# Kernel tuning notes

Measured on AMD Instinct MI355X. Metric: run time of the kernel, lower is better.

Reference implementation:

```python
import jax, jax.numpy as jnp
import numpy as np

BS, NQ, D = 4, 12500, 256
HEADS, LEVELS, POINTS = 8, 2, 4
HD = D // HEADS
D_FF = 2048
SHAPES = ((100, 100), (50, 50))   # (H, W) per level; sum(H*W) == NQ
STARTS = (0, 10000)


def layer_norm(x, g, b, eps=1e-5):
    m = x.mean(-1, keepdims=True)
    v = ((x - m) ** 2).mean(-1, keepdims=True)
    return (x - m) * jax.lax.rsqrt(v + eps) * g + b


def bilinear_sample(value_l, loc, H, W):
    # value_l: (bs, heads, H*W, hd); loc: (bs, heads, nq, P, 2) normalized [0,1]
    # matches F.grid_sample(align_corners=False, padding_mode='zeros')
    x = loc[..., 0] * W - 0.5
    y = loc[..., 1] * H - 0.5
    x0 = jnp.floor(x)
    y0 = jnp.floor(y)
    wx1 = x - x0
    wy1 = y - y0
    wx0 = 1.0 - wx1
    wy0 = 1.0 - wy1
    x0i = x0.astype(jnp.int32)
    y0i = y0.astype(jnp.int32)

    def gather(xi, yi):
        valid = (xi >= 0) & (xi < W) & (yi >= 0) & (yi < H)
        idx = jnp.clip(yi, 0, H - 1) * W + jnp.clip(xi, 0, W - 1)  # (bs,heads,nq,P)
        b, h, nq, P = idx.shape
        g = jnp.take_along_axis(value_l, idx.reshape(b, h, nq * P, 1), axis=2)
        g = g.reshape(b, h, nq, P, -1)
        return g * valid[..., None].astype(g.dtype)

    g00 = gather(x0i, y0i)
    g10 = gather(x0i + 1, y0i)
    g01 = gather(x0i, y0i + 1)
    g11 = gather(x0i + 1, y0i + 1)
    return (g00 * (wx0 * wy0)[..., None] + g10 * (wx1 * wy0)[..., None]
            + g01 * (wx0 * wy1)[..., None] + g11 * (wx1 * wy1)[..., None])


def setup_inputs() -> dict:
    key = jax.random.key(0)
    ks = jax.random.split(key, 20)
    s = 0.02
    inp = {
        'query': jax.random.normal(ks[0], (BS, NQ, D), jnp.float32),
        'reference_points': jax.random.uniform(ks[1], (BS, NQ, LEVELS, 2), jnp.float32),
        'w_off': s * jax.random.normal(ks[2], (D, HEADS * LEVELS * POINTS * 2), jnp.float32),
        'b_off': s * jax.random.normal(ks[3], (HEADS * LEVELS * POINTS * 2,), jnp.float32),
        'w_attn': s * jax.random.normal(ks[4], (D, HEADS * LEVELS * POINTS), jnp.float32),
        'b_attn': s * jax.random.normal(ks[5], (HEADS * LEVELS * POINTS,), jnp.float32),
        'w_val': s * jax.random.normal(ks[6], (D, D), jnp.float32),
        'b_val': jnp.zeros((D,), jnp.float32),
        'w_out': s * jax.random.normal(ks[7], (D, D), jnp.float32),
        'b_out': jnp.zeros((D,), jnp.float32),
        'w1': s * jax.random.normal(ks[8], (D, D_FF), jnp.float32),
        'b1': jnp.zeros((D_FF,), jnp.float32),
        'w2': s * jax.random.normal(ks[9], (D_FF, D), jnp.float32),
        'b2': jnp.zeros((D,), jnp.float32),
        'ln0_g': jnp.ones((D,), jnp.float32),
        'ln0_b': jnp.zeros((D,), jnp.float32),
        'ln1_g': jnp.ones((D,), jnp.float32),
        'ln1_b': jnp.zeros((D,), jnp.float32),
    }
    return inp


def reference(query, reference_points, w_off, b_off, w_attn, b_attn, w_val, b_val,
              w_out, b_out, w1, b1, w2, b2, ln0_g, ln0_b, ln1_g, ln1_b):
    bs, nq, _ = query.shape
    # value projection; encoder self-attention: value == query tokens
    value = (query @ w_val + b_val).reshape(bs, nq, HEADS, HD).transpose(0, 2, 1, 3)  # (bs,heads,nv,hd)
    off = (query @ w_off + b_off).reshape(bs, nq, HEADS, LEVELS, POINTS, 2)
    aw = (query @ w_attn + b_attn).reshape(bs, nq, HEADS, LEVELS * POINTS)
    aw = jax.nn.softmax(aw, axis=-1).reshape(bs, nq, HEADS, LEVELS, POINTS)

    out = jnp.zeros((bs, HEADS, nq, HD), query.dtype)
    for l, (H, W) in enumerate(SHAPES):
        normalizer = jnp.array([W, H], query.dtype)
        # (bs,nq,heads,P,2)
        loc = reference_points[:, :, None, l, None, :] + off[:, :, :, l] / normalizer
        loc = loc.transpose(0, 2, 1, 3, 4)  # (bs,heads,nq,P,2)
        v_l = value[:, :, STARTS[l]:STARTS[l] + H * W]  # (bs,heads,H*W,hd)
        sampled = bilinear_sample(v_l, loc, H, W)       # (bs,heads,nq,P,hd)
        w_l = aw[:, :, :, l].transpose(0, 2, 1, 3)      # (bs,heads,nq,P)
        out = out + (sampled * w_l[..., None]).sum(axis=3)

    attn_out = out.transpose(0, 2, 1, 3).reshape(bs, nq, D) @ w_out + b_out
    x = layer_norm(query + attn_out, ln0_g, ln0_b)
    h = jax.nn.relu(x @ w1 + b1)
    x = layer_norm(x + (h @ w2 + b2), ln1_g, ln1_b)
    return x
```

## Files before the change

### kernel.cpp

```cpp
#include <hip/hip_runtime.h>


#define NQv 12500
#define BSv 4
#define Dv  256
#define DFF 2048

typedef __attribute__((ext_vector_type(8))) __bf16 bf16x8;
typedef __attribute__((ext_vector_type(4))) float f32x4;

__device__ __forceinline__ ushort f32_to_bf16(float f) {
  unsigned u = __float_as_uint(f);
  u += 0x7FFFu + ((u >> 16) & 1u);
  return (ushort)(u >> 16);
}
__device__ __forceinline__ float bf16_to_f32(ushort u) {
  return __uint_as_float(((unsigned)u) << 16);
}

__global__ __launch_bounds__(256) void conv_bf16_kernel(
    const float* __restrict__ in, ushort* __restrict__ out, int n4) {
  int i = blockIdx.x * 256 + threadIdx.x;
  if (i >= n4) return;
  float4 v = reinterpret_cast<const float4*>(in)[i];
  uint2 st;
  st.x = (unsigned)f32_to_bf16(v.x) | ((unsigned)f32_to_bf16(v.y) << 16);
  st.y = (unsigned)f32_to_bf16(v.z) | ((unsigned)f32_to_bf16(v.w) << 16);
  reinterpret_cast<uint2*>(out)[i] = st;
}

__global__ __launch_bounds__(256) void ttrans_kernel(
    const float* __restrict__ in, ushort* __restrict__ out, int K, int N) {
  __shared__ ushort tl[64][65];
  const int n0 = blockIdx.x * 64, k0 = blockIdx.y * 64;
  const int t = threadIdx.x;
#pragma unroll
  for (int i = 0; i < 16; ++i) {
    int idx = t + 256 * i;
    int r = idx >> 6, c = idx & 63;
    tl[r][c] = f32_to_bf16(in[(size_t)(k0 + r) * N + n0 + c]);
  }
  __syncthreads();
#pragma unroll
  for (int i = 0; i < 16; ++i) {
    int idx = t + 256 * i;
    int r = idx >> 6, c = idx & 63;
    out[(size_t)(n0 + r) * K + k0 + c] = tl[c][r];
  }
}

__global__ __launch_bounds__(256) void build_wcat_kernel(
    const float* __restrict__ w_val, const float* __restrict__ w_off,
    const float* __restrict__ w_attn, const float* __restrict__ b_val,
    const float* __restrict__ b_off, const float* __restrict__ b_attn,
    ushort* __restrict__ wcat, float* __restrict__ bcat) {
  int i = blockIdx.x * 256 + threadIdx.x;
  if (i < 448 * 256) {
    int n = i >> 8, k = i & 255;
    float v = (n < 256) ? w_val[(size_t)k * 256 + n]
              : (n < 384) ? w_off[(size_t)k * 128 + (n - 256)]
                          : w_attn[(size_t)k * 64 + (n - 384)];
    wcat[i] = f32_to_bf16(v);
  }
  if (i < 512)
    bcat[i] = (i < 256) ? b_val[i] : (i < 384) ? b_off[i - 256]
              : (i < 448) ? b_attn[i - 384] : 0.f;
}

#define TBM 128
#define TBN 128
#define TBK 32

template <int RELU, int NMASK>
__global__ __launch_bounds__(256) void gemm128_kernel(
    const ushort* __restrict__ A, const ushort* __restrict__ Bt,
    const float* __restrict__ bias, ushort* __restrict__ C,
    int M, int K, int ldc, int Nreal) {
  __shared__ ushort lds[4][TBM * TBK];

  const int t = threadIdx.x;
  const int wid = t >> 6, lane = t & 63;
  const int wr = wid >> 1, wc = wid & 1;
  const int m0 = blockIdx.y * TBM;
  const int n0 = blockIdx.x * TBN;

  int srowA[2], srowB[2], gsl[2];
#pragma unroll
  for (int i = 0; i < 2; i++) {
    int row = i * 64 + (t >> 2);
    int ar = m0 + row;
    srowA[i] = (ar < M) ? ar : (M - 1);
    srowB[i] = n0 + row;
    gsl[i] = ((t & 3) ^ ((row >> 1) & 3)) * 8;
  }

  f32x4 acc[4][4] = {};
  const int nt = K / TBK;
  int cur = 0;

#pragma unroll
  for (int i = 0; i < 2; i++) {
    const int ldsoff = (i * 256 + wid * 64) * 8;
    __builtin_amdgcn_global_load_lds(
        (const __attribute__((address_space(1))) void*)(A + (size_t)srowA[i] * K + gsl[i]),
        (__attribute__((address_space(3))) void*)(lds[0] + ldsoff), 16, 0, 0);
    __builtin_amdgcn_global_load_lds(
        (const __attribute__((address_space(1))) void*)(Bt + (size_t)srowB[i] * K + gsl[i]),
        (__attribute__((address_space(3))) void*)(lds[1] + ldsoff), 16, 0, 0);
  }
  __syncthreads();

  const int rl = lane & 15, kh = lane >> 4;
  for (int tk = 0; tk < nt; ++tk) {
    if (tk + 1 < nt) {
      const int k0 = (tk + 1) * TBK;
      const int nb = (cur ^ 1) * 2;
#pragma unroll
      for (int i = 0; i < 2; i++) {
        const int ldsoff = (i * 256 + wid * 64) * 8;
        __builtin_amdgcn_global_load_lds(
            (const __attribute__((address_space(1))) void*)(A + (size_t)srowA[i] * K + k0 + gsl[i]),
            (__attribute__((address_space(3))) void*)(lds[nb] + ldsoff), 16, 0, 0);
        __builtin_amdgcn_global_load_lds(
            (const __attribute__((address_space(1))) void*)(Bt + (size_t)srowB[i] * K + k0 + gsl[i]),
            (__attribute__((address_space(3))) void*)(lds[nb + 1] + ldsoff), 16, 0, 0);
      }
    }
    {
      const ushort* As = lds[cur * 2];
      const ushort* Bs = lds[cur * 2 + 1];
      bf16x8 afr[4], bfr[4];
#pragma unroll
      for (int ni = 0; ni < 4; ni++) {
        int rowb = wc * 64 + ni * 16 + rl;
        int p = kh ^ ((rowb >> 1) & 3);
        bfr[ni] = *reinterpret_cast<const bf16x8*>(Bs + rowb * 32 + p * 8);
      }
#pragma unroll
      for (int mi = 0; mi < 4; mi++) {
        int rowa = wr * 64 + mi * 16 + rl;
        int p = kh ^ ((rowa >> 1) & 3);
        afr[mi] = *reinterpret_cast<const bf16x8*>(As + rowa * 32 + p * 8);
      }
#pragma unroll
      for (int mi = 0; mi < 4; mi++)
#pragma unroll
        for (int ni = 0; ni < 4; ni++)
          acc[mi][ni] = __builtin_amdgcn_mfma_f32_16x16x32_bf16(afr[mi], bfr[ni], acc[mi][ni], 0, 0, 0);
    }
    __syncthreads();
    cur ^= 1;
  }

  ushort* ldsC = lds[0];
  const int rgrp = lane >> 4, cl = lane & 15;
#pragma unroll
  for (int pass = 0; pass < 2; ++pass) {
    if (wr == pass) {
#pragma unroll
      for (int mi = 0; mi < 4; mi++) {
#pragma unroll
        for (int ni = 0; ni < 4; ni++) {
          int col = wc * 64 + ni * 16 + cl;
          float bv = bias[n0 + col];
#pragma unroll
          for (int r = 0; r < 4; r++) {
            int rloc = mi * 16 + rgrp * 4 + r;
            float v = acc[mi][ni][r] + bv;
            if (RELU) v = fmaxf(v, 0.f);
            ldsC[rloc * 132 + col] = f32_to_bf16(v);
          }
        }
      }
    }
    __syncthreads();
    {
      int rloc = t >> 2;
      int row = m0 + pass * 64 + rloc;
      if (row < M) {
#pragma unroll
        for (int j = 0; j < 4; j++) {
          int col = (t & 3) * 32 + j * 8;
          if (!NMASK || n0 + col < Nreal) {
            uint4 v = *reinterpret_cast<const uint4*>(ldsC + rloc * 132 + col);
            *reinterpret_cast<uint4*>(C + (size_t)row * ldc + n0 + col) = v;
          }
        }
      }
    }
    __syncthreads();
  }
}

__global__ __launch_bounds__(256, 2) void ffn_ln_fused_kernel(
    const ushort* __restrict__ xb,
    const ushort* __restrict__ w1t,
    const float* __restrict__ b1,
    const ushort* __restrict__ w2t,
    const float* __restrict__ b2,
    const float* __restrict__ g1, const float* __restrict__ be1,
    float* __restrict__ out,
    int M) {
  __shared__ ushort lds_all[40960];
  ushort* As  = lds_all;
  ushort* Hs  = lds_all + 16384;
  ushort* stg[2] = {lds_all + 24576, lds_all + 32768};
  float* zbuf = (float*)(lds_all + 16384);

  const int t = threadIdx.x;
  const int wv = t >> 6, lane = t & 63;
  const int rl = lane & 15, kq = lane >> 4;
  const int g = lane >> 4, cl = lane & 15;
  const int m0 = blockIdx.x * 64;

  const int r1 = t >> 3;
  const int ls1 = (t & 7) ^ (r1 & 7);
  const int r2 = t >> 2;
  const int ls2 = (t & 3) ^ ((t >> 3) & 3);
  const int rA = t >> 5;
  const int lsA = (t & 31) ^ ((t >> 5) & 7);

#pragma unroll
  for (int ii = 0; ii < 8; ++ii) {
    int row = rA + 8 * ii;
    int ar = m0 + row; ar = (ar < M) ? ar : (M - 1);
    __builtin_amdgcn_global_load_lds(
        (const __attribute__((address_space(1))) void*)(xb + (size_t)ar * 256 + lsA * 8),
        (__attribute__((address_space(3))) void*)(As + (t + 256 * ii) * 8), 16, 0, 0);
  }
#pragma unroll
  for (int ii = 0; ii < 4; ++ii) {
    __builtin_amdgcn_global_load_lds(
        (const __attribute__((address_space(1))) void*)(w1t + (size_t)(r1 + 32 * ii) * 256 + ls1 * 8),
        (__attribute__((address_space(3))) void*)(stg[0] + (t + 256 * ii) * 8), 16, 0, 0);
  }
  __syncthreads();

  auto issue_stage = [&](int i, ushort* dst) {
    int p = i >> 3, j = i & 7;
    if (j < 4) {
      const ushort* gp = w1t + (size_t)(p * 128 + r1) * 256 + j * 64 + ls1 * 8;
#pragma unroll
      for (int ii = 0; ii < 4; ++ii)
        __builtin_amdgcn_global_load_lds(
            (const __attribute__((address_space(1))) void*)(gp + (size_t)ii * 32 * 256),
            (__attribute__((address_space(3))) void*)(dst + (t + 256 * ii) * 8), 16, 0, 0);
    } else {
      const ushort* gp = w2t + (size_t)r2 * 2048 + p * 128 + (j - 4) * 32 + ls2 * 8;
#pragma unroll
      for (int ii = 0; ii < 4; ++ii)
        __builtin_amdgcn_global_load_lds(
            (const __attribute__((address_space(1))) void*)(gp + (size_t)ii * 64 * 2048),
            (__attribute__((address_space(3))) void*)(dst + (t + 256 * ii) * 8), 16, 0, 0);
    }
  };

  f32x4 acc1[4][2] = {};
  f32x4 accF[4][4] = {};
  int cur = 0;

  for (int p = 0; p < 16; ++p) {
#pragma unroll
    for (int j = 0; j < 4; ++j) {
      issue_stage(p * 8 + j + 1, stg[cur ^ 1]);
      const ushort* Bs = stg[cur];
#pragma unroll
      for (int kk = 0; kk < 2; ++kk) {
        bf16x8 afr[4], bfr[2];
        int slotA = j * 8 + kk * 4 + kq;
#pragma unroll
        for (int mi = 0; mi < 4; mi++) {
          int rowa = mi * 16 + rl;
          afr[mi] = *reinterpret_cast<const bf16x8*>(As + rowa * 256 + (slotA ^ (rowa & 7)) * 8);
        }
        int slotB = kk * 4 + kq;
#pragma unroll
        for (int ni = 0; ni < 2; ni++) {
          int rowb = wv * 32 + ni * 16 + rl;
          bfr[ni] = *reinterpret_cast<const bf16x8*>(Bs + rowb * 64 + (slotB ^ (rowb & 7)) * 8);
        }
#pragma unroll
        for (int mi = 0; mi < 4; mi++)
#pragma unroll
          for (int ni = 0; ni < 2; ni++)
            acc1[mi][ni] = __builtin_amdgcn_mfma_f32_16x16x32_bf16(afr[mi], bfr[ni], acc1[mi][ni], 0, 0, 0);
      }
      if (j == 3) {
#pragma unroll
        for (int ni = 0; ni < 2; ni++) {
          int col = wv * 32 + ni * 16 + cl;
          float b1v = b1[p * 128 + col];
#pragma unroll
          for (int mi = 0; mi < 4; mi++) {
#pragma unroll
            for (int r = 0; r < 4; r++) {
              int row = mi * 16 + g * 4 + r;
              float v = fmaxf(acc1[mi][ni][r] + b1v, 0.f);
              int phys = (col >> 3) ^ ((row >> 1) & 7);
              Hs[row * 128 + phys * 8 + (col & 7)] = f32_to_bf16(v);
            }
          }
        }
#pragma unroll
        for (int mi = 0; mi < 4; mi++)
#pragma unroll
          for (int ni = 0; ni < 2; ni++)
            acc1[mi][ni] = (f32x4){0.f, 0.f, 0.f, 0.f};
      }
      __syncthreads();
      cur ^= 1;
    }
#pragma unroll
    for (int tt = 0; tt < 4; ++tt) {
      int i = p * 8 + 4 + tt;
      if (i + 1 < 128) issue_stage(i + 1, stg[cur ^ 1]);
      const ushort* Bs = stg[cur];
      bf16x8 afr[4], bfr[4];
#pragma unroll
      for (int mi = 0; mi < 4; mi++) {
        int rowa = mi * 16 + rl;
        int slot = tt * 4 + kq;
        afr[mi] = *reinterpret_cast<const bf16x8*>(Hs + rowa * 128 + ((slot ^ ((rowa >> 1) & 7))) * 8);
      }
#pragma unroll
      for (int ni = 0; ni < 4; ni++) {
        int rowb = wv * 64 + ni * 16 + rl;
        bfr[ni] = *reinterpret_cast<const bf16x8*>(Bs + rowb * 32 + ((kq ^ ((rowb >> 1) & 3))) * 8);
      }
#pragma unroll
      for (int mi = 0; mi < 4; mi++)
#pragma unroll
        for (int ni = 0; ni < 4; ni++)
          accF[mi][ni] = __builtin_amdgcn_mfma_f32_16x16x32_bf16(afr[mi], bfr[ni], accF[mi][ni], 0, 0, 0);
      __syncthreads();
      cur ^= 1;
    }
  }

#pragma unroll
  for (int half = 0; half < 2; ++half) {
#pragma unroll
    for (int mm = 0; mm < 2; ++mm) {
      int mi = half * 2 + mm;
#pragma unroll
      for (int ni = 0; ni < 4; ni++) {
        int col = wv * 64 + ni * 16 + cl;
        float b2v = b2[col];
#pragma unroll
        for (int r = 0; r < 4; r++) {
          int rloc = mm * 16 + g * 4 + r;
          zbuf[rloc * 260 + col] = accF[mi][ni][r] + b2v;
        }
      }
    }
    __syncthreads();
#pragma unroll
    for (int it = 0; it < 8; ++it) {
      int rloc = wv * 8 + it;
      int rowt = half * 32 + rloc;
      float4 zv = *reinterpret_cast<const float4*>(&zbuf[rloc * 260 + lane * 4]);
      int phys = (lane >> 1) ^ (rowt & 7);
      const ushort* xp = As + rowt * 256 + phys * 8 + (lane & 1) * 4;
      float x0 = zv.x + bf16_to_f32(xp[0]);
      float x1 = zv.y + bf16_to_f32(xp[1]);
      float x2 = zv.z + bf16_to_f32(xp[2]);
      float x3 = zv.w + bf16_to_f32(xp[3]);
      float s = x0 + x1 + x2 + x3;
      float sq = x0 * x0 + x1 * x1 + x2 * x2 + x3 * x3;
#pragma unroll
      for (int o = 1; o < 64; o <<= 1) {
        s += __shfl_xor(s, o, 64);
        sq += __shfl_xor(sq, o, 64);
      }
      float mean = s * (1.f / 256.f);
      float var = sq * (1.f / 256.f) - mean * mean;
      float rs = rsqrtf(var + 1e-5f);
      float4 gv = *reinterpret_cast<const float4*>(g1 + lane * 4);
      float4 bv = *reinterpret_cast<const float4*>(be1 + lane * 4);
      float4 o4;
      o4.x = (x0 - mean) * rs * gv.x + bv.x;
      o4.y = (x1 - mean) * rs * gv.y + bv.y;
      o4.z = (x2 - mean) * rs * gv.z + bv.z;
      o4.w = (x3 - mean) * rs * gv.w + bv.w;
      int grow = m0 + rowt;
      if (grow < M)
        *reinterpret_cast<float4*>(out + (size_t)grow * 256 + lane * 4) = o4;
    }
    __syncthreads();
  }
}

__global__ __launch_bounds__(256) void deform_attn_kernel(
    const ushort* __restrict__ pcat, const float* __restrict__ refp,
    ushort* __restrict__ out, int total) {
  int tid = blockIdx.x * 256 + threadIdx.x;
  if (tid >= total) return;
  int c0 = (tid & 3) * 8;
  int idx = tid >> 2;
  int h = idx & 7;
  int row = idx >> 3;
  int bl = row / NQv;

  const ushort* prow = pcat + (size_t)row * 448;

  ushort awr[8];
  *reinterpret_cast<uint4*>(awr) = *reinterpret_cast<const uint4*>(prow + 384 + h * 8);
  float lg[8], mx = -1e30f;
#pragma unroll
  for (int i = 0; i < 8; i++) { lg[i] = bf16_to_f32(awr[i]); mx = fmaxf(mx, lg[i]); }
  float ssum = 0.f;
#pragma unroll
  for (int i = 0; i < 8; i++) { lg[i] = __expf(lg[i] - mx); ssum += lg[i]; }
  float inv = 1.f / ssum;

  ushort ofr[16];
  *reinterpret_cast<uint4*>(ofr)     = *reinterpret_cast<const uint4*>(prow + 256 + h * 16);
  *reinterpret_cast<uint4*>(ofr + 8) = *reinterpret_cast<const uint4*>(prow + 256 + h * 16 + 8);
  float4 rp = *reinterpret_cast<const float4*>(refp + (size_t)row * 4);

  float acc8[8] = {};
  const int Ws[2] = {100, 50}, Hs2[2] = {100, 50}, Ss[2] = {0, 10000};
#pragma unroll
  for (int l = 0; l < 2; l++) {
    const int W = Ws[l], H = Hs2[l];
    float fx = (l ? rp.z : rp.x) * (float)W - 0.5f;
    float fy = (l ? rp.w : rp.y) * (float)H - 0.5f;
    const ushort* vbase = pcat + ((size_t)bl * NQv + Ss[l]) * 448 + h * 32 + c0;
#pragma unroll
    for (int p = 0; p < 4; p++) {
      float x = fx + bf16_to_f32(ofr[l * 8 + p * 2 + 0]);
      float y = fy + bf16_to_f32(ofr[l * 8 + p * 2 + 1]);
      float x0f = floorf(x), y0f = floorf(y);
      float wx1 = x - x0f, wy1 = y - y0f;
      float wx0 = 1.f - wx1, wy0 = 1.f - wy1;
      int x0 = (int)x0f, y0 = (int)y0f;
      float aw = lg[l * 4 + p] * inv;

      float cw[4] = {aw * wx0 * wy0, aw * wx1 * wy0, aw * wx0 * wy1, aw * wx1 * wy1};
      int cx[4] = {x0, x0 + 1, x0, x0 + 1};
      int cy[4] = {y0, y0, y0 + 1, y0 + 1};
#pragma unroll
      for (int c = 0; c < 4; c++) {
        int xi = cx[c], yi = cy[c];
        if (xi >= 0 && xi < W && yi >= 0 && yi < H) {
          ushort vr[8];
          *reinterpret_cast<uint4*>(vr) =
              *reinterpret_cast<const uint4*>(vbase + (size_t)(yi * W + xi) * 448);
          float w = cw[c];
#pragma unroll
          for (int j = 0; j < 8; j++) acc8[j] += w * bf16_to_f32(vr[j]);
        }
      }
    }
  }

  ushort st[8];
#pragma unroll
  for (int j = 0; j < 8; j++) st[j] = f32_to_bf16(acc8[j]);
  *reinterpret_cast<uint4*>(out + (size_t)row * 256 + h * 32 + c0) =
      *reinterpret_cast<uint4*>(st);
}

__global__ __launch_bounds__(256) void ln0_kernel(
    const float* __restrict__ A, const ushort* __restrict__ B,
    const float* __restrict__ gamma, const float* __restrict__ beta,
    ushort* __restrict__ outb, int M) {
  int row = blockIdx.x * 4 + (threadIdx.x >> 6);
  int lane = threadIdx.x & 63;
  if (row >= M) return;
  size_t base = (size_t)row * 256 + lane * 4;
  float4 a = *reinterpret_cast<const float4*>(A + base);
  uint2 braw = *reinterpret_cast<const uint2*>(B + base);
  float x0 = a.x + bf16_to_f32((ushort)(braw.x & 0xffffu));
  float x1 = a.y + bf16_to_f32((ushort)(braw.x >> 16));
  float x2 = a.z + bf16_to_f32((ushort)(braw.y & 0xffffu));
  float x3 = a.w + bf16_to_f32((ushort)(braw.y >> 16));
  float s = x0 + x1 + x2 + x3;
  float sq = x0 * x0 + x1 * x1 + x2 * x2 + x3 * x3;
#pragma unroll
  for (int o = 1; o < 64; o <<= 1) {
    s += __shfl_xor(s, o, 64);
    sq += __shfl_xor(sq, o, 64);
  }
  float mean = s * (1.f / 256.f);
  float var = sq * (1.f / 256.f) - mean * mean;
  float rs = rsqrtf(var + 1e-5f);
  float4 gv = *reinterpret_cast<const float4*>(gamma + lane * 4);
  float4 bv = *reinterpret_cast<const float4*>(beta + lane * 4);
  float o0 = (x0 - mean) * rs * gv.x + bv.x;
  float o1 = (x1 - mean) * rs * gv.y + bv.y;
  float o2 = (x2 - mean) * rs * gv.z + bv.z;
  float o3 = (x3 - mean) * rs * gv.w + bv.w;
  uint2 st;
  st.x = (unsigned)f32_to_bf16(o0) | ((unsigned)f32_to_bf16(o1) << 16);
  st.y = (unsigned)f32_to_bf16(o2) | ((unsigned)f32_to_bf16(o3) << 16);
  *reinterpret_cast<uint2*>(outb + base) = st;
}

extern "C" void kernel_launch(void* const* d_in, const int* in_sizes, int n_in,
                              void* d_out, int out_size, void* d_ws, size_t ws_size,
                              hipStream_t stream) {
  const float* query  = (const float*)d_in[0];
  const float* refp   = (const float*)d_in[1];
  const float* w_off  = (const float*)d_in[2];
  const float* b_off  = (const float*)d_in[3];
  const float* w_attn = (const float*)d_in[4];
  const float* b_attn = (const float*)d_in[5];
  const float* w_val  = (const float*)d_in[6];
  const float* b_val  = (const float*)d_in[7];
  const float* w_out  = (const float*)d_in[8];
  const float* b_out  = (const float*)d_in[9];
  const float* w1     = (const float*)d_in[10];
  const float* b1     = (const float*)d_in[11];
  const float* w2     = (const float*)d_in[12];
  const float* b2     = (const float*)d_in[13];
  const float* ln0g   = (const float*)d_in[14];
  const float* ln0b   = (const float*)d_in[15];
  const float* ln1g   = (const float*)d_in[16];
  const float* ln1b   = (const float*)d_in[17];
  float* outp = (float*)d_out;

  char* ws = (char*)d_ws;
  size_t woff = 0;
  auto walloc = [&](size_t bytes) { size_t r = woff; woff += (bytes + 255) & ~(size_t)255; return r; };
  ushort* wcat = (ushort*)(ws + walloc((size_t)512 * 256 * 2));
  float*  bcat = (float*)(ws + walloc(512 * 4));
  ushort* wqt  = (ushort*)(ws + walloc((size_t)256 * 256 * 2));
  ushort* w1t  = (ushort*)(ws + walloc((size_t)DFF * 256 * 2));
  ushort* w2t  = (ushort*)(ws + walloc((size_t)256 * DFF * 2));
  char* arena = ws + woff;
  size_t arena_sz = (ws_size > woff) ? (ws_size - woff) : 0;

  int nb = ((size_t)BSv * NQv * 1920 + (1u << 20) <= arena_sz) ? BSv : 1;
  const int R = nb * NQv;
  ushort* qb   = (ushort*)arena;
  ushort* pcat = (ushort*)(arena + (size_t)R * 512);
  ushort* samp = (ushort*)(arena + (size_t)R * 1408);
  ushort* proj = qb;
  ushort* xb   = samp;

  build_wcat_kernel<<<dim3(448), dim3(256), 0, stream>>>(
      w_val, w_off, w_attn, b_val, b_off, b_attn, wcat, bcat);
  ttrans_kernel<<<dim3(4, 4), dim3(256), 0, stream>>>(w_out, wqt, Dv, Dv);
  ttrans_kernel<<<dim3(DFF / 64, 4), dim3(256), 0, stream>>>(w1, w1t, Dv, DFF);
  ttrans_kernel<<<dim3(4, DFF / 64), dim3(256), 0, stream>>>(w2, w2t, DFF, Dv);

  const int MT = (R + TBM - 1) / TBM;

  for (int c = 0; c < BSv / nb; c++) {
    const int row0 = c * R;
    const float* qrow = query + (size_t)row0 * Dv;

    conv_bf16_kernel<<<dim3((R * 64 + 255) / 256), dim3(256), 0, stream>>>(qrow, qb, R * 64);

    gemm128_kernel<0, 1><<<dim3(4, MT), dim3(256), 0, stream>>>(
        qb, wcat, bcat, pcat, R, Dv, 448, 448);

    deform_attn_kernel<<<dim3((R * 32 + 255) / 256), dim3(256), 0, stream>>>(
        pcat, refp + (size_t)row0 * 4, samp, R * 32);

    gemm128_kernel<0, 0><<<dim3(2, MT), dim3(256), 0, stream>>>(
        samp, wqt, b_out, proj, R, Dv, 256, 256);

    ln0_kernel<<<dim3((R + 3) / 4), dim3(256), 0, stream>>>(qrow, proj, ln0g, ln0b, xb, R);

    ffn_ln_fused_kernel<<<dim3((R + 63) / 64), dim3(256), 0, stream>>>(
        xb, w1t, b1, w2t, b2, ln1g, ln1b, outp + (size_t)row0 * 256, R);
  }
}
```

Measured before the change: 339.7 us.

## Restructure fused FFN kernel to 128-row tiles with triple-buffered weight staging

```diff
diff --git a/kernel.cpp b/kernel.cpp
--- a/kernel.cpp
+++ b/kernel.cpp
@@ -192,7 +192,7 @@
   }
 }
 
-__global__ __launch_bounds__(256, 2) void ffn_ln_fused_kernel(
+__global__ __launch_bounds__(512, 1) void ffn_ln_fused_kernel(
     const ushort* __restrict__ xb,
     const ushort* __restrict__ w1t,
     const float* __restrict__ b1,
@@ -201,59 +201,59 @@
     const float* __restrict__ g1, const float* __restrict__ be1,
     float* __restrict__ out,
     int M) {
-  __shared__ ushort lds_all[40960];
-  ushort* As  = lds_all;
-  ushort* Hs  = lds_all + 16384;
-  ushort* stg[2] = {lds_all + 24576, lds_all + 32768};
-  float* zbuf = (float*)(lds_all + 16384);
+  __shared__ ushort lds_all[74752];
+  ushort* As = lds_all;
+  ushort* Hs = lds_all + 32768;
+  ushort* stg0 = lds_all + 50176;
 
   const int t = threadIdx.x;
-  const int wv = t >> 6, lane = t & 63;
+  const int wv = t >> 6;
+  const int wm = wv >> 2;
+  const int wn = wv & 3;
+  const int lane = t & 63;
   const int rl = lane & 15, kq = lane >> 4;
-  const int g = lane >> 4, cl = lane & 15;
-  const int m0 = blockIdx.x * 64;
-
-  const int r1 = t >> 3;
-  const int ls1 = (t & 7) ^ (r1 & 7);
-  const int r2 = t >> 2;
-  const int ls2 = (t & 3) ^ ((t >> 3) & 3);
-  const int rA = t >> 5;
-  const int lsA = (t & 31) ^ ((t >> 5) & 7);
+  const int cl = lane & 15, g4 = lane >> 4;
+  const int m0 = blockIdx.x * 128;
+
+  const int b1row = t >> 3, b1slot = t & 7;
+  const int b2row = t >> 2, b2slot = t & 3;
+
+  auto stg = [&](int i) { return stg0 + i * 8192; };
+
+  auto issueB1 = [&](int p, int j, ushort* dst) {
+#pragma unroll
+    for (int ii = 0; ii < 2; ++ii) {
+      int row = b1row + 64 * ii;
+      int g = b1slot ^ (row & 7);
+      __builtin_amdgcn_global_load_lds(
+          (const __attribute__((address_space(1))) void*)(
+              w1t + (size_t)(p * 128 + row) * 256 + j * 64 + g * 8),
+          (__attribute__((address_space(3))) void*)(dst + (t + 512 * ii) * 8), 16, 0, 0);
+    }
+  };
+  auto issueB2 = [&](int p, int tt, ushort* dst) {
+#pragma unroll
+    for (int ii = 0; ii < 2; ++ii) {
+      int row = b2row + 128 * ii;
+      int g = b2slot ^ ((row >> 1) & 3);
+      __builtin_amdgcn_global_load_lds(
+          (const __attribute__((address_space(1))) void*)(
+              w2t + (size_t)row * 2048 + p * 128 + tt * 32 + g * 8),
+          (__attribute__((address_space(3))) void*)(dst + (t + 512 * ii) * 8), 16, 0, 0);
+    }
+  };
 
 #pragma unroll
   for (int ii = 0; ii < 8; ++ii) {
-    int row = rA + 8 * ii;
+    int row = (t >> 5) + 16 * ii;
+    int g = (t & 31) ^ (row & 7);
     int ar = m0 + row; ar = (ar < M) ? ar : (M - 1);
     __builtin_amdgcn_global_load_lds(
-        (const __attribute__((address_space(1))) void*)(xb + (size_t)ar * 256 + lsA * 8),
-        (__attribute__((address_space(3))) void*)(As + (t + 256 * ii) * 8), 16, 0, 0);
-  }
-#pragma unroll
-  for (int ii = 0; ii < 4; ++ii) {
-    __builtin_amdgcn_global_load_lds(
-        (const __attribute__((address_space(1))) void*)(w1t + (size_t)(r1 + 32 * ii) * 256 + ls1 * 8),
-        (__attribute__((address_space(3))) void*)(stg[0] + (t + 256 * ii) * 8), 16, 0, 0);
-  }
-  __syncthreads();
-
-  auto issue_stage = [&](int i, ushort* dst) {
-    int p = i >> 3, j = i & 7;
-    if (j < 4) {
-      const ushort* gp = w1t + (size_t)(p * 128 + r1) * 256 + j * 64 + ls1 * 8;
-#pragma unroll
-      for (int ii = 0; ii < 4; ++ii)
-        __builtin_amdgcn_global_load_lds(
-            (const __attribute__((address_space(1))) void*)(gp + (size_t)ii * 32 * 256),
-            (__attribute__((address_space(3))) void*)(dst + (t + 256 * ii) * 8), 16, 0, 0);
-    } else {
-      const ushort* gp = w2t + (size_t)r2 * 2048 + p * 128 + (j - 4) * 32 + ls2 * 8;
-#pragma unroll
-      for (int ii = 0; ii < 4; ++ii)
-        __builtin_amdgcn_global_load_lds(
-            (const __attribute__((address_space(1))) void*)(gp + (size_t)ii * 64 * 2048),
-            (__attribute__((address_space(3))) void*)(dst + (t + 256 * ii) * 8), 16, 0, 0);
-    }
-  };
+        (const __attribute__((address_space(1))) void*)(xb + (size_t)ar * 256 + g * 8),
+        (__attribute__((address_space(3))) void*)(As + (t + 512 * ii) * 8), 16, 0, 0);
+  }
+  issueB1(0, 0, stg(0));
+  issueB1(0, 1, stg(1));
 
   f32x4 acc1[4][2] = {};
   f32x4 accF[4][4] = {};
@@ -261,132 +261,167 @@
 
   for (int p = 0; p < 16; ++p) {
 #pragma unroll
-    for (int j = 0; j < 4; ++j) {
-      issue_stage(p * 8 + j + 1, stg[cur ^ 1]);
-      const ushort* Bs = stg[cur];
-#pragma unroll
-      for (int kk = 0; kk < 2; ++kk) {
-        bf16x8 afr[4], bfr[2];
-        int slotA = j * 8 + kk * 4 + kq;
-#pragma unroll
-        for (int mi = 0; mi < 4; mi++) {
-          int rowa = mi * 16 + rl;
-          afr[mi] = *reinterpret_cast<const bf16x8*>(As + rowa * 256 + (slotA ^ (rowa & 7)) * 8);
-        }
-        int slotB = kk * 4 + kq;
-#pragma unroll
-        for (int ni = 0; ni < 2; ni++) {
-          int rowb = wv * 32 + ni * 16 + rl;
-          bfr[ni] = *reinterpret_cast<const bf16x8*>(Bs + rowb * 64 + (slotB ^ (rowb & 7)) * 8);
-        }
-#pragma unroll
-        for (int mi = 0; mi < 4; mi++)
-#pragma unroll
-          for (int ni = 0; ni < 2; ni++)
-            acc1[mi][ni] = __builtin_amdgcn_mfma_f32_16x16x32_bf16(afr[mi], bfr[ni], acc1[mi][ni], 0, 0, 0);
-      }
-      if (j == 3) {
-#pragma unroll
-        for (int ni = 0; ni < 2; ni++) {
-          int col = wv * 32 + ni * 16 + cl;
-          float b1v = b1[p * 128 + col];
+    for (int j = 0; j < 8; ++j) {
+      int tgt = cur + 2; if (tgt >= 3) tgt -= 3;
+      if (j <= 5) {
+        const int j2 = j + 2;
+        const int p2 = p + (j2 >> 3);
+        if ((j2 & 7) < 4) issueB1(p2, j2 & 3, stg(tgt));
+        else issueB2(p2, (j2 & 7) - 4, stg(tgt));
+        asm volatile("s_waitcnt vmcnt(4) lgkmcnt(0)" ::: "memory");
+      } else if (p < 15) {
+        const int j2m = (j + 2) & 7;
+        issueB1(p + 1, j2m, stg(tgt));
+        asm volatile("s_waitcnt vmcnt(4) lgkmcnt(0)" ::: "memory");
+      } else if (j == 6) {
+        asm volatile("s_waitcnt vmcnt(2) lgkmcnt(0)" ::: "memory");
+      } else {
+        asm volatile("s_waitcnt vmcnt(0) lgkmcnt(0)" ::: "memory");
+      }
+      __builtin_amdgcn_s_barrier();
+      __builtin_amdgcn_sched_barrier(0);
+
+      const ushort* Bs = stg(cur);
+      if (j < 4) {
+        __builtin_amdgcn_s_setprio(1);
+#pragma unroll
+        for (int kk = 0; kk < 2; ++kk) {
+          bf16x8 afr[4], bfr[2];
+          const int slotA = j * 8 + kk * 4 + kq;
 #pragma unroll
           for (int mi = 0; mi < 4; mi++) {
-#pragma unroll
-            for (int r = 0; r < 4; r++) {
-              int row = mi * 16 + g * 4 + r;
-              float v = fmaxf(acc1[mi][ni][r] + b1v, 0.f);
-              int phys = (col >> 3) ^ ((row >> 1) & 7);
-              Hs[row * 128 + phys * 8 + (col & 7)] = f32_to_bf16(v);
+            int rowa = wm * 64 + mi * 16 + rl;
+            afr[mi] = *reinterpret_cast<const bf16x8*>(As + rowa * 256 + (slotA ^ (rowa & 7)) * 8);
+          }
+          const int slotB = kk * 4 + kq;
+#pragma unroll
+          for (int ni = 0; ni < 2; ni++) {
+            int rowb = wn * 32 + ni * 16 + rl;
+            bfr[ni] = *reinterpret_cast<const bf16x8*>(Bs + rowb * 64 + (slotB ^ (rowb & 7)) * 8);
+          }
+#pragma unroll
+          for (int mi = 0; mi < 4; mi++)
+#pragma unroll
+            for (int ni = 0; ni < 2; ni++)
+              acc1[mi][ni] = __builtin_amdgcn_mfma_f32_16x16x32_bf16(afr[mi], bfr[ni], acc1[mi][ni], 0, 0, 0);
+        }
+        __builtin_amdgcn_s_setprio(0);
+        if (j == 3) {
+#pragma unroll
+          for (int ni = 0; ni < 2; ni++) {
+            int col = wn * 32 + ni * 16 + cl;
+            float b1v = b1[p * 128 + col];
+#pragma unroll
+            for (int mi = 0; mi < 4; mi++) {
+#pragma unroll
+              for (int r = 0; r < 4; r++) {
+                int row = wm * 64 + mi * 16 + g4 * 4 + r;
+                Hs[row * 136 + col] = f32_to_bf16(fmaxf(acc1[mi][ni][r] + b1v, 0.f));
+              }
             }
           }
-        }
+#pragma unroll
+          for (int mi = 0; mi < 4; mi++)
+#pragma unroll
+            for (int ni = 0; ni < 2; ni++)
+              acc1[mi][ni] = (f32x4){0.f, 0.f, 0.f, 0.f};
+        }
+      } else {
+        const int tt = j - 4;
+        bf16x8 afr[4], bfr[4];
+#pragma unroll
+        for (int mi = 0; mi < 4; mi++) {
+          int rowa = wm * 64 + mi * 16 + rl;
+          afr[mi] = *reinterpret_cast<const bf16x8*>(Hs + rowa * 136 + (tt * 4 + kq) * 8);
+        }
+#pragma unroll
+        for (int ni = 0; ni < 4; ni++) {
+          int rowb = wn * 64 + ni * 16 + rl;
+          bfr[ni] = *reinterpret_cast<const bf16x8*>(Bs + rowb * 32 + (kq ^ ((rowb >> 1) & 3)) * 8);
+        }
+        __builtin_amdgcn_s_setprio(1);
 #pragma unroll
         for (int mi = 0; mi < 4; mi++)
 #pragma unroll
-          for (int ni = 0; ni < 2; ni++)
-            acc1[mi][ni] = (f32x4){0.f, 0.f, 0.f, 0.f};
-      }
-      __syncthreads();
-      cur ^= 1;
-    }
-#pragma unroll
-    for (int tt = 0; tt < 4; ++tt) {
-      int i = p * 8 + 4 + tt;
-      if (i + 1 < 128) issue_stage(i + 1, stg[cur ^ 1]);
-      const ushort* Bs = stg[cur];
-      bf16x8 afr[4], bfr[4];
-#pragma unroll
-      for (int mi = 0; mi < 4; mi++) {
-        int rowa = mi * 16 + rl;
-        int slot = tt * 4 + kq;
-        afr[mi] = *reinterpret_cast<const bf16x8*>(Hs + rowa * 128 + ((slot ^ ((rowa >> 1) & 7))) * 8);
-      }
-#pragma unroll
-      for (int ni = 0; ni < 4; ni++) {
-        int rowb = wv * 64 + ni * 16 + rl;
-        bfr[ni] = *reinterpret_cast<const bf16x8*>(Bs + rowb * 32 + ((kq ^ ((rowb >> 1) & 3))) * 8);
-      }
-#pragma unroll
-      for (int mi = 0; mi < 4; mi++)
-#pragma unroll
-        for (int ni = 0; ni < 4; ni++)
-          accF[mi][ni] = __builtin_amdgcn_mfma_f32_16x16x32_bf16(afr[mi], bfr[ni], accF[mi][ni], 0, 0, 0);
-      __syncthreads();
-      cur ^= 1;
-    }
-  }
-
-#pragma unroll
-  for (int half = 0; half < 2; ++half) {
-#pragma unroll
-    for (int mm = 0; mm < 2; ++mm) {
-      int mi = half * 2 + mm;
-#pragma unroll
-      for (int ni = 0; ni < 4; ni++) {
-        int col = wv * 64 + ni * 16 + cl;
-        float b2v = b2[col];
-#pragma unroll
-        for (int r = 0; r < 4; r++) {
-          int rloc = mm * 16 + g * 4 + r;
-          zbuf[rloc * 260 + col] = accF[mi][ni][r] + b2v;
-        }
-      }
-    }
-    __syncthreads();
-#pragma unroll
-    for (int it = 0; it < 8; ++it) {
-      int rloc = wv * 8 + it;
-      int rowt = half * 32 + rloc;
-      float4 zv = *reinterpret_cast<const float4*>(&zbuf[rloc * 260 + lane * 4]);
-      int phys = (lane >> 1) ^ (rowt & 7);
-      const ushort* xp = As + rowt * 256 + phys * 8 + (lane & 1) * 4;
-      float x0 = zv.x + bf16_to_f32(xp[0]);
-      float x1 = zv.y + bf16_to_f32(xp[1]);
-      float x2 = zv.z + bf16_to_f32(xp[2]);
-      float x3 = zv.w + bf16_to_f32(xp[3]);
-      float s = x0 + x1 + x2 + x3;
-      float sq = x0 * x0 + x1 * x1 + x2 * x2 + x3 * x3;
-#pragma unroll
-      for (int o = 1; o < 64; o <<= 1) {
+          for (int ni = 0; ni < 4; ni++)
+            accF[mi][ni] = __builtin_amdgcn_mfma_f32_16x16x32_bf16(afr[mi], bfr[ni], accF[mi][ni], 0, 0, 0);
+        __builtin_amdgcn_s_setprio(0);
+      }
+      cur = cur + 1; if (cur >= 3) cur -= 3;
+    }
+  }
+
+  float* ptab = (float*)stg0;
+  float* mtab = (float*)(stg0 + 2048);
+
+  float b2c[4], g1c[4], bec[4];
+#pragma unroll
+  for (int ni = 0; ni < 4; ni++) {
+    int col = wn * 64 + ni * 16 + cl;
+    b2c[ni] = b2[col]; g1c[ni] = g1[col]; bec[ni] = be1[col];
+  }
+#pragma unroll
+  for (int mi = 0; mi < 4; mi++) {
+#pragma unroll
+    for (int ni = 0; ni < 4; ni++) {
+      int col = wn * 64 + ni * 16 + cl;
+#pragma unroll
+      for (int r = 0; r < 4; r++) {
+        int row = wm * 64 + mi * 16 + g4 * 4 + r;
+        ushort xv = As[row * 256 + ((col >> 3) ^ (row & 7)) * 8 + (col & 7)];
+        accF[mi][ni][r] += b2c[ni] + bf16_to_f32(xv);
+      }
+    }
+  }
+#pragma unroll
+  for (int mi = 0; mi < 4; mi++) {
+#pragma unroll
+    for (int r = 0; r < 4; r++) {
+      float s = accF[mi][0][r] + accF[mi][1][r] + accF[mi][2][r] + accF[mi][3][r];
+      float sq = accF[mi][0][r] * accF[mi][0][r] + accF[mi][1][r] * accF[mi][1][r] +
+                 accF[mi][2][r] * accF[mi][2][r] + accF[mi][3][r] * accF[mi][3][r];
+#pragma unroll
+      for (int o = 1; o < 16; o <<= 1) {
         s += __shfl_xor(s, o, 64);
         sq += __shfl_xor(sq, o, 64);
       }
+      if (cl == 0) {
+        int row = wm * 64 + mi * 16 + g4 * 4 + r;
+        ptab[(row * 4 + wn) * 2 + 0] = s;
+        ptab[(row * 4 + wn) * 2 + 1] = sq;
+      }
+    }
+  }
+  __syncthreads();
+  {
+    int row = t >> 2, part = t & 3;
+    float s = ptab[(row * 4 + part) * 2 + 0];
+    float sq = ptab[(row * 4 + part) * 2 + 1];
+    s += __shfl_xor(s, 1, 64);  sq += __shfl_xor(sq, 1, 64);
+    s += __shfl_xor(s, 2, 64);  sq += __shfl_xor(sq, 2, 64);
+    if (part == 0) {
       float mean = s * (1.f / 256.f);
       float var = sq * (1.f / 256.f) - mean * mean;
-      float rs = rsqrtf(var + 1e-5f);
-      float4 gv = *reinterpret_cast<const float4*>(g1 + lane * 4);
-      float4 bv = *reinterpret_cast<const float4*>(be1 + lane * 4);
-      float4 o4;
-      o4.x = (x0 - mean) * rs * gv.x + bv.x;
-      o4.y = (x1 - mean) * rs * gv.y + bv.y;
-      o4.z = (x2 - mean) * rs * gv.z + bv.z;
-      o4.w = (x3 - mean) * rs * gv.w + bv.w;
-      int grow = m0 + rowt;
-      if (grow < M)
-        *reinterpret_cast<float4*>(out + (size_t)grow * 256 + lane * 4) = o4;
-    }
-    __syncthreads();
+      mtab[row * 2 + 0] = mean;
+      mtab[row * 2 + 1] = rsqrtf(var + 1e-5f);
+    }
+  }
+  __syncthreads();
+#pragma unroll
+  for (int mi = 0; mi < 4; mi++) {
+#pragma unroll
+    for (int r = 0; r < 4; r++) {
+      int row = wm * 64 + mi * 16 + g4 * 4 + r;
+      float2 ms = *reinterpret_cast<const float2*>(mtab + row * 2);
+      int grow = m0 + row;
+      if (grow < M) {
+#pragma unroll
+        for (int ni = 0; ni < 4; ni++) {
+          int col = wn * 64 + ni * 16 + cl;
+          out[(size_t)grow * 256 + col] = (accF[mi][ni][r] - ms.x) * ms.y * g1c[ni] + bec[ni];
+        }
+      }
+    }
   }
 }
 
@@ -564,7 +599,7 @@
 
     ln0_kernel<<<dim3((R + 3) / 4), dim3(256), 0, stream>>>(qrow, proj, ln0g, ln0b, xb, R);
 
-    ffn_ln_fused_kernel<<<dim3((R + 63) / 64), dim3(256), 0, stream>>>(
+    ffn_ln_fused_kernel<<<dim3((R + 127) / 128), dim3(512), 0, stream>>>(
         xb, w1t, b1, w2t, b2, ln1g, ln1b, outp + (size_t)row0 * 256, R);
   }
 }
```

New measurement: 338.4 us. No clear change (-0.4%).
